# Optimization experiments

Hardware: AMD Instinct MI355X
Metric: run time of the kernel (lower is better)

## Reference

```python
import jax, jax.numpy as jnp
import numpy as np

N, C, H, W = 2, 8, 256, 512
K = 9   # kernel_size
D = 1   # dilation


def setup_inputs() -> dict:
    key = jax.random.key(0)
    k1, k2, k3 = jax.random.split(key, 3)
    x_in = jax.random.normal(k1, (N, C, H, W), dtype=jnp.float32)
    filters = jax.random.normal(k2, (N, K * K, H, W), dtype=jnp.float32)
    filters_biases = jax.random.normal(k3, (N, 1, H, W), dtype=jnp.float32)
    return {"x_in": x_in, "filters": filters, "filters_biases": filters_biases}


def reference(x_in, filters, filters_biases):
    # Dynamic (per-pixel) filtering: out[n,c,h,w] = sum_{i,j} x_pad[n,c,h+i*d,w+j*d] * filters[n,i*K+j,h,w] + bias
    # Equivalent to torch: unfold -> [N,C,K*K,H,W], multiply by filters [N,1,K*K,H,W], sum over K*K, add bias.
    # Fused accumulation over the K*K taps avoids materializing the K*K-times larger im2col tensor.
    k, d = K, D
    p = d * (k - 1) // 2  # 'same' padding used by im2col_layer
    n, c, h, w = x_in.shape
    xp = jnp.pad(x_in, ((0, 0), (0, 0), (p, p), (p, p)))
    out = jnp.zeros_like(x_in)
    for i in range(k):          # fixed small kernel loop (81 taps), unrolled by jit
        for j in range(k):
            tap = filters[:, None, i * k + j]                  # [N,1,H,W]
            out = out + xp[:, :, i * d:i * d + h, j * d:j * d + w] * tap
    return out + filters_biases
```

## Files before the change

### kernel.cpp

```cpp
#include <hip/hip_runtime.h>

#define CC 8
#define HH 256
#define WW 512
#define KK 9
#define XF 268

__global__ __launch_bounds__(256) void dynfilter_kernel(
    const float* __restrict__ x,
    const float* __restrict__ filt,
    const float* __restrict__ fbias,
    float* __restrict__ out)
{
    __shared__ __align__(16) float xs[2][CC][XF];

    const int tid = threadIdx.x;
    const int bid = blockIdx.x;
    const int seg = bid & 1;
    const int h   = (bid >> 1) & 255;
    const int n   = bid >> 9;

    const int pxg = tid & 127;
    const int cg  = tid >> 7;
    const int w0  = seg * 256 + (pxg << 1);

    const int lane32  = tid & 31;
    const int cstage  = tid >> 5;
    const int wstage0 = seg * 256 - 4;
    const float* xcrow = x + ((size_t)(n * CC + cstage)) * ((size_t)HH * WW) + wstage0;

    const size_t HW = (size_t)HH * WW;
    const float* fptr = filt + ((size_t)(n * 81) * HH + h) * WW + w0;

    float acc[4][2];
    {
        const float2 fb = *(const float2*)(fbias + ((size_t)(n * HH + h)) * WW + w0);
        acc[0][0] = fb.x; acc[0][1] = fb.y;
        acc[1][0] = fb.x; acc[1][1] = fb.y;
        acc[2][0] = fb.x; acc[2][1] = fb.y;
        acc[3][0] = fb.x; acc[3][1] = fb.y;
    }

    {
        const int hh = h - 4;
        const bool rowok = (hh >= 0);
        const float* src = xcrow + (size_t)hh * WW;
        float4 s0 = make_float4(0.f,0.f,0.f,0.f), s1 = s0, s2 = s0;
        int w;
        w = wstage0 + (lane32 << 2);
        if (rowok && (unsigned)w < (unsigned)WW) s0 = *(const float4*)(src + (lane32 << 2));
        w = wstage0 + ((lane32 + 32) << 2);
        if (rowok && (unsigned)w < (unsigned)WW) s1 = *(const float4*)(src + ((lane32 + 32) << 2));
        w = wstage0 + ((lane32 + 64) << 2);
        if (lane32 < 2 && rowok && (unsigned)w < (unsigned)WW) s2 = *(const float4*)(src + ((lane32 + 64) << 2));
        *(float4*)&xs[0][cstage][lane32 << 2] = s0;
        *(float4*)&xs[0][cstage][(lane32 + 32) << 2] = s1;
        if (lane32 < 2) *(float4*)&xs[0][cstage][(lane32 + 64) << 2] = s2;
    }
    __syncthreads();

    #pragma clang loop unroll(disable)
    for (int i = 0; i < KK; ++i) {
        const int buf = i & 1;

        float2 f0, f1, f2, f3, f4, f5, f6, f7, f8;
        {
            const float* fi = fptr + (size_t)i * KK * HW;
            f0 = *(const float2*)(fi + 0 * HW);
            f1 = *(const float2*)(fi + 1 * HW);
            f2 = *(const float2*)(fi + 2 * HW);
            f3 = *(const float2*)(fi + 3 * HW);
            f4 = *(const float2*)(fi + 4 * HW);
            f5 = *(const float2*)(fi + 5 * HW);
            f6 = *(const float2*)(fi + 6 * HW);
            f7 = *(const float2*)(fi + 7 * HW);
            f8 = *(const float2*)(fi + 8 * HW);
        }

        float4 s0 = make_float4(0.f,0.f,0.f,0.f), s1 = s0, s2 = s0;
        if (i < KK - 1) {
            const int hh = h - 3 + i;
            const bool rowok = (unsigned)hh < (unsigned)HH;
            const float* src = xcrow + (size_t)hh * WW;
            int w;
            w = wstage0 + (lane32 << 2);
            if (rowok && (unsigned)w < (unsigned)WW) s0 = *(const float4*)(src + (lane32 << 2));
            w = wstage0 + ((lane32 + 32) << 2);
            if (rowok && (unsigned)w < (unsigned)WW) s1 = *(const float4*)(src + ((lane32 + 32) << 2));
            w = wstage0 + ((lane32 + 64) << 2);
            if (lane32 < 2 && rowok && (unsigned)w < (unsigned)WW) s2 = *(const float4*)(src + ((lane32 + 64) << 2));
        }

        #pragma unroll
        for (int c = 0; c < 4; ++c) {
            const float* xp = &xs[buf][(cg << 2) + c][pxg << 1];
            float2 v0 = *(const float2*)(xp + 0);
            float2 v1 = *(const float2*)(xp + 2);
            float2 v2 = *(const float2*)(xp + 4);
            float2 v3 = *(const float2*)(xp + 6);
            float2 v4 = *(const float2*)(xp + 8);
            float a0 = acc[c][0], a1 = acc[c][1];
            a0 = fmaf(f0.x, v0.x, a0);  a1 = fmaf(f0.y, v0.y, a1);
            a0 = fmaf(f1.x, v0.y, a0);  a1 = fmaf(f1.y, v1.x, a1);
            a0 = fmaf(f2.x, v1.x, a0);  a1 = fmaf(f2.y, v1.y, a1);
            a0 = fmaf(f3.x, v1.y, a0);  a1 = fmaf(f3.y, v2.x, a1);
            a0 = fmaf(f4.x, v2.x, a0);  a1 = fmaf(f4.y, v2.y, a1);
            a0 = fmaf(f5.x, v2.y, a0);  a1 = fmaf(f5.y, v3.x, a1);
            a0 = fmaf(f6.x, v3.x, a0);  a1 = fmaf(f6.y, v3.y, a1);
            a0 = fmaf(f7.x, v3.y, a0);  a1 = fmaf(f7.y, v4.x, a1);
            a0 = fmaf(f8.x, v4.x, a0);  a1 = fmaf(f8.y, v4.y, a1);
            acc[c][0] = a0; acc[c][1] = a1;
        }

        if (i < KK - 1) {
            *(float4*)&xs[buf ^ 1][cstage][lane32 << 2] = s0;
            *(float4*)&xs[buf ^ 1][cstage][(lane32 + 32) << 2] = s1;
            if (lane32 < 2) *(float4*)&xs[buf ^ 1][cstage][(lane32 + 64) << 2] = s2;
        }
        __syncthreads();
    }

    #pragma unroll
    for (int c = 0; c < 4; ++c) {
        *(float2*)(out + ((size_t)(n * CC + (cg << 2) + c) * HH + h) * WW + w0) =
            make_float2(acc[c][0], acc[c][1]);
    }
}

extern "C" void kernel_launch(void* const* d_in, const int* in_sizes, int n_in,
                              void* d_out, int out_size, void* d_ws, size_t ws_size,
                              hipStream_t stream) {
    const float* x  = (const float*)d_in[0];
    const float* f  = (const float*)d_in[1];
    const float* fb = (const float*)d_in[2];
    float* o = (float*)d_out;
    hipLaunchKernelGGL(dynfilter_kernel, dim3(1024), dim3(256), 0, stream,
                       x, f, fb, o);
}
```

Baseline: 137.3 us.

## Give each wavefront two channels and private LDS rows, dropping block barriers

Work is reorganized so each 64-lane wavefront owns two channels and computes four adjacent pixels per lane. It stages the x rows into its own double-buffered LDS slice, which removes every __syncthreads in the tap loop. Filter and bias loads widen to float4, and each lane reads 12 contiguous x values to serve 9 taps across 4 pixels. In exchange, all four wavefronts now load the same filter values, so filter traffic per block rises from 2x to 4x redundancy and relies on cache hits. Correctness depends on LDS operations staying ordered within a wavefront.

```diff
diff --git a/kernel.cpp b/kernel.cpp
--- a/kernel.cpp
+++ b/kernel.cpp
@@ -4,126 +4,124 @@
 #define HH 256
 #define WW 512
 #define KK 9
-#define XF 268
+#define XF 272
 
-__global__ __launch_bounds__(256) void dynfilter_kernel(
+__global__ __launch_bounds__(256, 4) void dynfilter_kernel(
     const float* __restrict__ x,
     const float* __restrict__ filt,
     const float* __restrict__ fbias,
     float* __restrict__ out)
 {
-    __shared__ __align__(16) float xs[2][CC][XF];
+    __shared__ __align__(16) float xs[4][2][2][XF];
 
-    const int tid = threadIdx.x;
+    const int tid  = threadIdx.x;
+    const int wv   = tid >> 6;
+    const int lane = tid & 63;
+
     const int bid = blockIdx.x;
     const int seg = bid & 1;
     const int h   = (bid >> 1) & 255;
     const int n   = bid >> 9;
 
-    const int pxg = tid & 127;
-    const int cg  = tid >> 7;
-    const int w0  = seg * 256 + (pxg << 1);
-
-    const int lane32  = tid & 31;
-    const int cstage  = tid >> 5;
+    const int w0      = seg * 256 + (lane << 2);
     const int wstage0 = seg * 256 - 4;
-    const float* xcrow = x + ((size_t)(n * CC + cstage)) * ((size_t)HH * WW) + wstage0;
 
     const size_t HW = (size_t)HH * WW;
+    const int c0 = wv << 1;
+
+    const float* xr0  = x + (size_t)(n * CC + c0)     * HW + wstage0;
+    const float* xr1  = x + (size_t)(n * CC + c0 + 1) * HW + wstage0;
     const float* fptr = filt + ((size_t)(n * 81) * HH + h) * WW + w0;
 
-    float acc[4][2];
+    float acc0[4], acc1[4];
     {
-        const float2 fb = *(const float2*)(fbias + ((size_t)(n * HH + h)) * WW + w0);
-        acc[0][0] = fb.x; acc[0][1] = fb.y;
-        acc[1][0] = fb.x; acc[1][1] = fb.y;
-        acc[2][0] = fb.x; acc[2][1] = fb.y;
-        acc[3][0] = fb.x; acc[3][1] = fb.y;
+        const float4 b4 = *(const float4*)(fbias + ((size_t)(n * HH + h)) * WW + w0);
+        acc0[0]=b4.x; acc0[1]=b4.y; acc0[2]=b4.z; acc0[3]=b4.w;
+        acc1[0]=b4.x; acc1[1]=b4.y; acc1[2]=b4.z; acc1[3]=b4.w;
     }
+
+    const int wlo = wstage0 + (lane << 2);
+    const int whi = wstage0 + 256 + (lane << 2);
+    const bool lo_ok = (unsigned)wlo < (unsigned)WW;
+    const bool hi_ok = (lane < 2) && ((unsigned)whi < (unsigned)WW);
 
     {
         const int hh = h - 4;
-        const bool rowok = (hh >= 0);
-        const float* src = xcrow + (size_t)hh * WW;
-        float4 s0 = make_float4(0.f,0.f,0.f,0.f), s1 = s0, s2 = s0;
-        int w;
-        w = wstage0 + (lane32 << 2);
-        if (rowok && (unsigned)w < (unsigned)WW) s0 = *(const float4*)(src + (lane32 << 2));
-        w = wstage0 + ((lane32 + 32) << 2);
-        if (rowok && (unsigned)w < (unsigned)WW) s1 = *(const float4*)(src + ((lane32 + 32) << 2));
-        w = wstage0 + ((lane32 + 64) << 2);
-        if (lane32 < 2 && rowok && (unsigned)w < (unsigned)WW) s2 = *(const float4*)(src + ((lane32 + 64) << 2));
-        *(float4*)&xs[0][cstage][lane32 << 2] = s0;
-        *(float4*)&xs[0][cstage][(lane32 + 32) << 2] = s1;
-        if (lane32 < 2) *(float4*)&xs[0][cstage][(lane32 + 64) << 2] = s2;
+        const bool rowok = hh >= 0;
+        const float* s0 = xr0 + (size_t)hh * WW;
+        const float* s1 = xr1 + (size_t)hh * WW;
+        float4 a0 = make_float4(0.f,0.f,0.f,0.f), b0 = a0, a1 = a0, b1 = a0;
+        if (rowok && lo_ok) { a0 = *(const float4*)(s0 + (lane<<2));       a1 = *(const float4*)(s1 + (lane<<2)); }
+        if (rowok && hi_ok) { b0 = *(const float4*)(s0 + 256 + (lane<<2)); b1 = *(const float4*)(s1 + 256 + (lane<<2)); }
+        *(float4*)&xs[wv][0][0][lane<<2] = a0;
+        *(float4*)&xs[wv][0][1][lane<<2] = a1;
+        if (lane < 2) {
+            *(float4*)&xs[wv][0][0][256 + (lane<<2)] = b0;
+            *(float4*)&xs[wv][0][1][256 + (lane<<2)] = b1;
+        }
     }
-    __syncthreads();
 
     #pragma clang loop unroll(disable)
     for (int i = 0; i < KK; ++i) {
         const int buf = i & 1;
 
-        float2 f0, f1, f2, f3, f4, f5, f6, f7, f8;
-        {
-            const float* fi = fptr + (size_t)i * KK * HW;
-            f0 = *(const float2*)(fi + 0 * HW);
-            f1 = *(const float2*)(fi + 1 * HW);
-            f2 = *(const float2*)(fi + 2 * HW);
-            f3 = *(const float2*)(fi + 3 * HW);
-            f4 = *(const float2*)(fi + 4 * HW);
-            f5 = *(const float2*)(fi + 5 * HW);
-            f6 = *(const float2*)(fi + 6 * HW);
-            f7 = *(const float2*)(fi + 7 * HW);
-            f8 = *(const float2*)(fi + 8 * HW);
-        }
-
-        float4 s0 = make_float4(0.f,0.f,0.f,0.f), s1 = s0, s2 = s0;
+        float4 a0 = make_float4(0.f,0.f,0.f,0.f), b0 = a0, a1 = a0, b1 = a0;
         if (i < KK - 1) {
             const int hh = h - 3 + i;
             const bool rowok = (unsigned)hh < (unsigned)HH;
-            const float* src = xcrow + (size_t)hh * WW;
-            int w;
-            w = wstage0 + (lane32 << 2);
-            if (rowok && (unsigned)w < (unsigned)WW) s0 = *(const float4*)(src + (lane32 << 2));
-            w = wstage0 + ((lane32 + 32) << 2);
-            if (rowok && (unsigned)w < (unsigned)WW) s1 = *(const float4*)(src + ((lane32 + 32) << 2));
-            w = wstage0 + ((lane32 + 64) << 2);
-            if (lane32 < 2 && rowok && (unsigned)w < (unsigned)WW) s2 = *(const float4*)(src + ((lane32 + 64) << 2));
+            const float* s0 = xr0 + (size_t)hh * WW;
+            const float* s1 = xr1 + (size_t)hh * WW;
+            if (rowok && lo_ok) { a0 = *(const float4*)(s0 + (lane<<2));       a1 = *(const float4*)(s1 + (lane<<2)); }
+            if (rowok && hi_ok) { b0 = *(const float4*)(s0 + 256 + (lane<<2)); b1 = *(const float4*)(s1 + 256 + (lane<<2)); }
+        }
+
+        float4 f[9];
+        {
+            const float* fi = fptr + (size_t)i * KK * HW;
+            #pragma unroll
+            for (int j = 0; j < 9; ++j) f[j] = *(const float4*)(fi + (size_t)j * HW);
+        }
+
+        float v0[12], v1[12];
+        {
+            const float* p0 = &xs[wv][buf][0][lane << 2];
+            const float* p1 = &xs[wv][buf][1][lane << 2];
+            float4 u;
+            u = *(const float4*)(p0 + 0); v0[0]=u.x; v0[1]=u.y; v0[2] =u.z; v0[3] =u.w;
+            u = *(const float4*)(p0 + 4); v0[4]=u.x; v0[5]=u.y; v0[6] =u.z; v0[7] =u.w;
+            u = *(const float4*)(p0 + 8); v0[8]=u.x; v0[9]=u.y; v0[10]=u.z; v0[11]=u.w;
+            u = *(const float4*)(p1 + 0); v1[0]=u.x; v1[1]=u.y; v1[2] =u.z; v1[3] =u.w;
+            u = *(const float4*)(p1 + 4); v1[4]=u.x; v1[5]=u.y; v1[6] =u.z; v1[7] =u.w;
+            u = *(const float4*)(p1 + 8); v1[8]=u.x; v1[9]=u.y; v1[10]=u.z; v1[11]=u.w;
         }
 
         #pragma unroll
-        for (int c = 0; c < 4; ++c) {
-            const float* xp = &xs[buf][(cg << 2) + c][pxg << 1];
-            float2 v0 = *(const float2*)(xp + 0);
-            float2 v1 = *(const float2*)(xp + 2);
-            float2 v2 = *(const float2*)(xp + 4);
-            float2 v3 = *(const float2*)(xp + 6);
-            float2 v4 = *(const float2*)(xp + 8);
-            float a0 = acc[c][0], a1 = acc[c][1];
-            a0 = fmaf(f0.x, v0.x, a0);  a1 = fmaf(f0.y, v0.y, a1);
-            a0 = fmaf(f1.x, v0.y, a0);  a1 = fmaf(f1.y, v1.x, a1);
-            a0 = fmaf(f2.x, v1.x, a0);  a1 = fmaf(f2.y, v1.y, a1);
-            a0 = fmaf(f3.x, v1.y, a0);  a1 = fmaf(f3.y, v2.x, a1);
-            a0 = fmaf(f4.x, v2.x, a0);  a1 = fmaf(f4.y, v2.y, a1);
-            a0 = fmaf(f5.x, v2.y, a0);  a1 = fmaf(f5.y, v3.x, a1);
-            a0 = fmaf(f6.x, v3.x, a0);  a1 = fmaf(f6.y, v3.y, a1);
-            a0 = fmaf(f7.x, v3.y, a0);  a1 = fmaf(f7.y, v4.x, a1);
-            a0 = fmaf(f8.x, v4.x, a0);  a1 = fmaf(f8.y, v4.y, a1);
-            acc[c][0] = a0; acc[c][1] = a1;
+        for (int j = 0; j < 9; ++j) {
+            acc0[0] = fmaf(f[j].x, v0[j+0], acc0[0]);
+            acc0[1] = fmaf(f[j].y, v0[j+1], acc0[1]);
+            acc0[2] = fmaf(f[j].z, v0[j+2], acc0[2]);
+            acc0[3] = fmaf(f[j].w, v0[j+3], acc0[3]);
+            acc1[0] = fmaf(f[j].x, v1[j+0], acc1[0]);
+            acc1[1] = fmaf(f[j].y, v1[j+1], acc1[1]);
+            acc1[2] = fmaf(f[j].z, v1[j+2], acc1[2]);
+            acc1[3] = fmaf(f[j].w, v1[j+3], acc1[3]);
         }
 
         if (i < KK - 1) {
-            *(float4*)&xs[buf ^ 1][cstage][lane32 << 2] = s0;
-            *(float4*)&xs[buf ^ 1][cstage][(lane32 + 32) << 2] = s1;
-            if (lane32 < 2) *(float4*)&xs[buf ^ 1][cstage][(lane32 + 64) << 2] = s2;
+            *(float4*)&xs[wv][buf ^ 1][0][lane<<2] = a0;
+            *(float4*)&xs[wv][buf ^ 1][1][lane<<2] = a1;
+            if (lane < 2) {
+                *(float4*)&xs[wv][buf ^ 1][0][256 + (lane<<2)] = b0;
+                *(float4*)&xs[wv][buf ^ 1][1][256 + (lane<<2)] = b1;
+            }
         }
-        __syncthreads();
     }
 
-    #pragma unroll
-    for (int c = 0; c < 4; ++c) {
-        *(float2*)(out + ((size_t)(n * CC + (cg << 2) + c) * HH + h) * WW + w0) =
-            make_float2(acc[c][0], acc[c][1]);
+    {
+        const float4 o0 = make_float4(acc0[0], acc0[1], acc0[2], acc0[3]);
+        const float4 o1 = make_float4(acc1[0], acc1[1], acc1[2], acc1[3]);
+        *(float4*)(out + ((size_t)(n * CC + c0)     * HH + h) * WW + w0) = o0;
+        *(float4*)(out + ((size_t)(n * CC + c0 + 1) * HH + h) * WW + w0) = o1;
     }
 }
 
```

After: 137.5 us. No clear change (+0.2%).
